# Optimization experiments

Measured on AMD Instinct MI355X. Metric: run time of the kernel, lower is better.

Reference implementation:

```python
import jax, jax.numpy as jnp
import numpy as np

D_MODEL = 1024
N_HEADS = 16
HEAD_DIM = D_MODEL // N_HEADS
NUM_SINK = 4
WINDOW = 512
B, S = 1, 4096


def _sink_visible(S):
    # visible[i, j] = (j <= i) & ((j < NUM_SINK) | (j >= i - WINDOW + 1))
    i = jnp.arange(S)[:, None]
    j = jnp.arange(S)[None, :]
    return (j <= i) & ((j < NUM_SINK) | (j >= i - WINDOW + 1))


def setup_inputs() -> dict:
    key = jax.random.key(0)
    kx, kq, kk, kv, ko = jax.random.split(key, 5)
    sc = 1.0 / np.sqrt(D_MODEL)
    return {
        "x": jax.random.normal(kx, (B, S, D_MODEL), dtype=jnp.float32),
        "Wq": jax.random.normal(kq, (D_MODEL, D_MODEL), dtype=jnp.float32) * sc,
        "Wk": jax.random.normal(kk, (D_MODEL, D_MODEL), dtype=jnp.float32) * sc,
        "Wv": jax.random.normal(kv, (D_MODEL, D_MODEL), dtype=jnp.float32) * sc,
        "Wo": jax.random.normal(ko, (D_MODEL, D_MODEL), dtype=jnp.float32) * sc,
    }


def reference(x, Wq, Wk, Wv, Wo):
    Bx, Sx, D = x.shape
    H, hd = N_HEADS, HEAD_DIM
    # nn.Linear (no bias): y = x @ W^T
    q = (x @ Wq.T).reshape(Bx, Sx, H, hd).transpose(0, 2, 1, 3)  # (B,H,S,hd)
    k = (x @ Wk.T).reshape(Bx, Sx, H, hd).transpose(0, 2, 1, 3)
    v = (x @ Wv.T).reshape(Bx, Sx, H, hd).transpose(0, 2, 1, 3)
    scale = 1.0 / np.sqrt(hd)
    scores = jnp.einsum("bhqd,bhkd->bhqk", q, k) * scale  # (B,H,S,S)
    visible = _sink_visible(Sx)  # (S,S) bool; every row has j=i visible
    scores = jnp.where(visible[None, None], scores, -jnp.inf)
    attn = jax.nn.softmax(scores, axis=-1)
    out = jnp.einsum("bhqk,bhkd->bhqd", attn, v)
    out = out.transpose(0, 2, 1, 3).reshape(Bx, Sx, D)
    return out @ Wo.T
```

## Files before the change

### kernel.cpp

```cpp
#include <hip/hip_runtime.h>
#include <stdint.h>

#define AS1 __attribute__((address_space(1)))
#define AS3 __attribute__((address_space(3)))

typedef short short8 __attribute__((ext_vector_type(8)));
typedef unsigned short ushort8 __attribute__((ext_vector_type(8)));
typedef __bf16 bf16x8 __attribute__((ext_vector_type(8)));
typedef float floatx4 __attribute__((ext_vector_type(4)));

__device__ __forceinline__ floatx4 mfma16(short8 a, short8 b, floatx4 c) {
  return __builtin_amdgcn_mfma_f32_16x16x32_bf16(
      __builtin_bit_cast(bf16x8, a), __builtin_bit_cast(bf16x8, b), c, 0, 0, 0);
}

__device__ __forceinline__ unsigned short f2bf(float f) {
  uint32_t u = __builtin_bit_cast(uint32_t, f);
  u = (u + 0x7FFFu + ((u >> 16) & 1u)) >> 16;
  return (unsigned short)u;
}

__device__ __forceinline__ uint32_t cvt_pk_bf16(float a, float b) {
  uint32_t d;
  asm("v_cvt_pk_bf16_f32 %0, %1, %2" : "=v"(d) : "v"(a), "v"(b));
  return d;
}

__global__ __launch_bounds__(256) void convert_pack(
    const float4* __restrict__ x, const float4* __restrict__ wq,
    const float4* __restrict__ wk, const float4* __restrict__ wv,
    const float4* __restrict__ wo, ushort4* __restrict__ xb,
    ushort4* __restrict__ wqkvb, ushort4* __restrict__ wob) {
  int i = blockIdx.x * 256 + threadIdx.x;
  const float4* src;
  ushort4* dst;
  if (i < (1 << 20)) {
    src = x + i;
    dst = xb + i;
  } else {
    int t = i - (1 << 20);
    int r = t >> 18;
    int j = t & ((1 << 18) - 1);
    src = (r == 0 ? wq : r == 1 ? wk : r == 2 ? wv : wo) + j;
    dst = (r < 3) ? (wqkvb + (r << 18) + j) : (wob + j);
  }
  float4 v = *src;
  ushort4 o;
  o.x = f2bf(v.x);
  o.y = f2bf(v.y);
  o.z = f2bf(v.z);
  o.w = f2bf(v.w);
  *dst = o;
}

template <typename OutT>
__global__ __launch_bounds__(256) void gemm_bt(const unsigned short* __restrict__ A,
                                               const unsigned short* __restrict__ Bm,
                                               OutT* __restrict__ C, int N, int K) {
  __shared__ unsigned short lds[3][16 * 512];
  const int tid = threadIdx.x;
  const int lane = tid & 63;
  const int w = tid >> 6;
  const int wr = w >> 1, wc = w & 1;

  const int lid = blockIdx.y * gridDim.x + blockIdx.x;
  const int xcd = lid & 7;
  const int wgid = xcd * 96 + (lid >> 3);
  const int s = wgid >> 5, w5 = wgid & 31;
  const int mt = (s & 3) * 8 + (w5 & 7);
  const int nt = (s >> 2) * 4 + (w5 >> 3);
  const int tm = mt * 128, tn = nt * 128;
  const int lrow = lane & 15;
  const int lk = (lane >> 4) * 8;

  floatx4 acc[4][4];
#pragma unroll
  for (int i = 0; i < 4; ++i)
#pragma unroll
    for (int j = 0; j < 4; ++j) acc[i][j] = floatx4{0.f, 0.f, 0.f, 0.f};

  auto stage = [&](unsigned short* buf, int k0) {
#pragma unroll
    for (int c = w * 4; c < w * 4 + 4; ++c) {
      const unsigned short* g;
      if (c < 8) {
        g = A + (size_t)(tm + c * 16 + lrow) * K + (k0 + lk);
      } else {
        g = Bm + (size_t)(tn + (c - 8) * 16 + lrow) * K + (k0 + lk);
      }
      __builtin_amdgcn_global_load_lds((const AS1 uint32_t*)g,
                                       (AS3 uint32_t*)(buf + c * 512), 16, 0, 0);
    }
  };

  auto compute = [&](const unsigned short* L) {
    short8 af[4], bf[4];
#pragma unroll
    for (int i = 0; i < 4; ++i)
      af[i] = *(const short8*)&L[(wr * 4 + i) * 512 + lane * 8];
#pragma unroll
    for (int j = 0; j < 4; ++j)
      bf[j] = *(const short8*)&L[(8 + wc * 4 + j) * 512 + lane * 8];
#pragma unroll
    for (int i = 0; i < 4; ++i)
#pragma unroll
      for (int j = 0; j < 4; ++j) acc[i][j] = mfma16(af[i], bf[j], acc[i][j]);
  };

  stage(lds[0], 0);
  stage(lds[1], 32);

  const int T = K >> 5;
  int bt = 0;
  for (int t = 0; t < T - 1; ++t) {
    asm volatile("s_waitcnt vmcnt(4)" ::: "memory");
    __builtin_amdgcn_sched_barrier(0);
    __builtin_amdgcn_s_barrier();
    __builtin_amdgcn_sched_barrier(0);
    if (t + 2 < T) {
      int b2 = (bt + 2 >= 3) ? bt - 1 : bt + 2;
      stage(lds[b2], (t + 2) << 5);
    }
    compute(lds[bt]);
    bt = (bt + 1 == 3) ? 0 : bt + 1;
  }
  asm volatile("s_waitcnt vmcnt(0)" ::: "memory");
  __builtin_amdgcn_sched_barrier(0);
  __builtin_amdgcn_s_barrier();
  __builtin_amdgcn_sched_barrier(0);
  compute(lds[bt]);

  const int r0 = (lane >> 4) * 4;
#pragma unroll
  for (int i = 0; i < 4; ++i)
#pragma unroll
    for (int j = 0; j < 4; ++j)
#pragma unroll
      for (int r = 0; r < 4; ++r) {
        int row = tm + wr * 64 + i * 16 + r0 + r;
        int col = tn + wc * 64 + j * 16 + lrow;
        float v = acc[i][j][r];
        if constexpr (sizeof(OutT) == 2)
          C[(size_t)row * N + col] = f2bf(v);
        else
          C[(size_t)row * N + col] = v;
      }
}

__global__ __launch_bounds__(256) void gemm64(const unsigned short* __restrict__ A,
                                              const unsigned short* __restrict__ Bm,
                                              float* __restrict__ C, int N, int K) {
  __shared__ unsigned short lds[3][12 * 512];
  const int tid = threadIdx.x;
  const int lane = tid & 63;
  const int w = tid >> 6;
  const int wr = w >> 1, wc = w & 1;

  const int lid = blockIdx.y * gridDim.x + blockIdx.x;
  const int xcd = lid & 7;
  const int wgid = xcd * 64 + (lid >> 3);
  const int s = wgid >> 5, w5 = wgid & 31;
  const int mt = (s & 3) * 16 + (w5 & 15);
  const int nt = (s >> 2) * 2 + (w5 >> 4);
  const int tm = mt * 64, tn = nt * 128;
  const int lrow = lane & 15;
  const int lk = (lane >> 4) * 8;

  floatx4 acc[2][4];
#pragma unroll
  for (int i = 0; i < 2; ++i)
#pragma unroll
    for (int j = 0; j < 4; ++j) acc[i][j] = floatx4{0.f, 0.f, 0.f, 0.f};

  auto stage = [&](unsigned short* buf, int k0) {
#pragma unroll
    for (int c = w * 3; c < w * 3 + 3; ++c) {
      const unsigned short* g;
      if (c < 4) {
        g = A + (size_t)(tm + c * 16 + lrow) * K + (k0 + lk);
      } else {
        g = Bm + (size_t)(tn + (c - 4) * 16 + lrow) * K + (k0 + lk);
      }
      __builtin_amdgcn_global_load_lds((const AS1 uint32_t*)g,
                                       (AS3 uint32_t*)(buf + c * 512), 16, 0, 0);
    }
  };

  auto compute = [&](const unsigned short* L) {
    short8 af[2], bf[4];
#pragma unroll
    for (int i = 0; i < 2; ++i)
      af[i] = *(const short8*)&L[(wr * 2 + i) * 512 + lane * 8];
#pragma unroll
    for (int j = 0; j < 4; ++j)
      bf[j] = *(const short8*)&L[(4 + wc * 4 + j) * 512 + lane * 8];
#pragma unroll
    for (int i = 0; i < 2; ++i)
#pragma unroll
      for (int j = 0; j < 4; ++j) acc[i][j] = mfma16(af[i], bf[j], acc[i][j]);
  };

  stage(lds[0], 0);
  stage(lds[1], 32);

  const int T = K >> 5;
  int bt = 0;
  for (int t = 0; t < T - 1; ++t) {
    asm volatile("s_waitcnt vmcnt(3)" ::: "memory");
    __builtin_amdgcn_sched_barrier(0);
    __builtin_amdgcn_s_barrier();
    __builtin_amdgcn_sched_barrier(0);
    if (t + 2 < T) {
      int b2 = (bt + 2 >= 3) ? bt - 1 : bt + 2;
      stage(lds[b2], (t + 2) << 5);
    }
    compute(lds[bt]);
    bt = (bt + 1 == 3) ? 0 : bt + 1;
  }
  asm volatile("s_waitcnt vmcnt(0)" ::: "memory");
  __builtin_amdgcn_sched_barrier(0);
  __builtin_amdgcn_s_barrier();
  __builtin_amdgcn_sched_barrier(0);
  compute(lds[bt]);

  const int r0 = (lane >> 4) * 4;
#pragma unroll
  for (int i = 0; i < 2; ++i)
#pragma unroll
    for (int j = 0; j < 4; ++j)
#pragma unroll
      for (int r = 0; r < 4; ++r) {
        int row = tm + (wr * 2 + i) * 16 + r0 + r;
        int col = tn + (wc * 4 + j) * 16 + lrow;
        C[(size_t)row * N + col] = acc[i][j][r];
      }
}

__global__ __launch_bounds__(256) void attn_kernel(const unsigned short* __restrict__ qkv,
                                                   unsigned short* __restrict__ aout) {
  __shared__ unsigned short Klds[2][16 * 512];
  __shared__ unsigned short VT[64 * 136];
  __shared__ unsigned short PT[4][16 * 136];

  const int tid = threadIdx.x;
  const int lane = tid & 63;
  const int w = tid >> 6;
  const int lrow = lane & 15;
  const int lkg = lane >> 4;

  const int i = blockIdx.x;
  const int half = i >> 8;
  const int j = (i >> 3) & 31;
  const int h = 2 * (i & 7) + half;
  const int qb = half ? (31 - j) : j;
  const int q0 = qb * 128;

  short8 qf[2][2];
#pragma unroll
  for (int qt = 0; qt < 2; ++qt)
#pragma unroll
    for (int ks = 0; ks < 2; ++ks)
      qf[qt][ks] = *(const short8*)&qkv[(size_t)(q0 + qt * 64 + w * 16 + lrow) * 3072 +
                                        h * 64 + ks * 32 + lkg * 8];

  float m_i[2], l_i[2];
  floatx4 o[4][2];
#pragma unroll
  for (int qt = 0; qt < 2; ++qt) {
    m_i[qt] = -1e30f;
    l_i[qt] = 0.f;
#pragma unroll
    for (int nt = 0; nt < 4; ++nt) o[nt][qt] = floatx4{0.f, 0.f, 0.f, 0.f};
  }

  const float scale2 = 0.125f * 1.44269504088896f;

  if (w < 2) {
    const unsigned short* g = &qkv[(size_t)lrow * 3072 + 1024 + h * 64 + w * 32 + lkg * 8];
    __builtin_amdgcn_global_load_lds((const AS1 uint32_t*)g,
                                     (AS3 uint32_t*)(&Klds[0][w * 512]), 16, 0, 0);
  }
  {
    if (lane < 16) {
      const unsigned short* g0 = &qkv[(size_t)(2 * lane) * 3072 + 2048 + h * 64 + w * 16];
      ushort8 a0 = *(const ushort8*)g0;
      ushort8 a1 = *(const ushort8*)(g0 + 8);
      ushort8 b0 = *(const ushort8*)(g0 + 3072);
      ushort8 b1 = *(const ushort8*)(g0 + 3080);
      uint32_t* vt = (uint32_t*)VT;
#pragma unroll
      for (int dd = 0; dd < 8; ++dd) {
        vt[(w * 16 + dd) * 68 + lane] = (uint32_t)a0[dd] | ((uint32_t)b0[dd] << 16);
        vt[(w * 16 + 8 + dd) * 68 + lane] = (uint32_t)a1[dd] | ((uint32_t)b1[dd] << 16);
      }
    }
  }
  const int kb0 = (q0 - 511 < 16) ? 16 : (q0 - 511);
#pragma unroll
  for (int c = 0; c < 4; ++c) {
    int ch = w * 4 + c;
    int kt = ch >> 1, ks = ch & 1;
    const unsigned short* g =
        &qkv[(size_t)(kb0 + kt * 16 + lrow) * 3072 + 1024 + h * 64 + ks * 32 + lkg * 8];
    __builtin_amdgcn_global_load_lds((const AS1 uint32_t*)g,
                                     (AS3 uint32_t*)(&Klds[1][ch * 512]), 16, 0, 0);
  }
  ushort8 va0, va1, vb0, vb1;
  {
    const unsigned short* g0 = &qkv[(size_t)(kb0 + 2 * lane) * 3072 + 2048 + h * 64 + w * 16];
    va0 = *(const ushort8*)g0;
    va1 = *(const ushort8*)(g0 + 8);
    vb0 = *(const ushort8*)(g0 + 3072);
    vb1 = *(const ushort8*)(g0 + 3080);
  }
  __syncthreads();

#pragma unroll
  for (int qt = 0; qt < 2; ++qt) {
    const int qq = q0 + qt * 64 + w * 16 + lrow;
    floatx4 s0 = floatx4{0.f, 0.f, 0.f, 0.f};
#pragma unroll
    for (int ks = 0; ks < 2; ++ks) {
      short8 kf = *(const short8*)&Klds[0][ks * 512 + lane * 8];
      s0 = mfma16(kf, qf[qt][ks], s0);
    }
    float mx = -1e30f;
    float sv[4];
#pragma unroll
    for (int r = 0; r < 4; ++r) {
      int key = lkg * 4 + r;
      bool vis = (key <= qq) && ((key < 4) || (key >= qq - 511));
      sv[r] = vis ? s0[r] * scale2 : -1e30f;
      mx = fmaxf(mx, sv[r]);
    }
    mx = fmaxf(mx, __shfl_xor(mx, 16));
    mx = fmaxf(mx, __shfl_xor(mx, 32));
    m_i[qt] = mx;
    float p0 = exp2f(sv[0] - mx), p1 = exp2f(sv[1] - mx);
    float p2 = exp2f(sv[2] - mx), p3 = exp2f(sv[3] - mx);
    float ps = (p0 + p1) + (p2 + p3);
    *(uint2*)&PT[w][lrow * 136 + lkg * 4] = uint2{cvt_pk_bf16(p0, p1), cvt_pk_bf16(p2, p3)};
    *(uint2*)&PT[w][lrow * 136 + 16 + lkg * 4] = uint2{0u, 0u};
    ps += __shfl_xor(ps, 16);
    ps += __shfl_xor(ps, 32);
    l_i[qt] = ps;
    short8 pf = *(const short8*)&PT[w][lrow * 136 + lkg * 8];
#pragma unroll
    for (int nt = 0; nt < 4; ++nt) {
      short8 vf = *(const short8*)&VT[(nt * 16 + lrow) * 136 + lkg * 8];
      o[nt][qt] = mfma16(vf, pf, o[nt][qt]);
    }
  }

  int nbuf = 1;
  for (int kb = kb0; kb < q0 + 128; kb += 128) {
    const bool hasnext = (kb + 128 < q0 + 128);
    __syncthreads();
    {
      uint32_t* vt = (uint32_t*)VT;
#pragma unroll
      for (int dd = 0; dd < 8; ++dd) {
        vt[(w * 16 + dd) * 68 + lane] = (uint32_t)va0[dd] | ((uint32_t)vb0[dd] << 16);
        vt[(w * 16 + 8 + dd) * 68 + lane] = (uint32_t)va1[dd] | ((uint32_t)vb1[dd] << 16);
      }
    }
    __syncthreads();

    if (hasnext) {
      const int kn = kb + 128;
#pragma unroll
      for (int c = 0; c < 4; ++c) {
        int ch = w * 4 + c;
        int kt = ch >> 1, ks = ch & 1;
        const unsigned short* g =
            &qkv[(size_t)(kn + kt * 16 + lrow) * 3072 + 1024 + h * 64 + ks * 32 + lkg * 8];
        __builtin_amdgcn_global_load_lds((const AS1 uint32_t*)g,
                                         (AS3 uint32_t*)(&Klds[1 - nbuf][ch * 512]), 16, 0, 0);
      }
      const unsigned short* g0 = &qkv[(size_t)(kn + 2 * lane) * 3072 + 2048 + h * 64 + w * 16];
      va0 = *(const ushort8*)g0;
      va1 = *(const ushort8*)(g0 + 8);
      vb0 = *(const ushort8*)(g0 + 3072);
      vb1 = *(const ushort8*)(g0 + 3080);
    }

#pragma unroll
    for (int qt = 0; qt < 2; ++qt) {
      const int qaT = q0 + qt * 64 + w * 16;
      const int qq = qaT + lrow;
      floatx4 s[8];
#pragma unroll
      for (int ct = 0; ct < 8; ++ct) {
        s[ct] = floatx4{0.f, 0.f, 0.f, 0.f};
#pragma unroll
        for (int ks = 0; ks < 2; ++ks) {
          short8 kf = *(const short8*)&Klds[nbuf][(ct * 2 + ks) * 512 + lane * 8];
          s[ct] = mfma16(kf, qf[qt][ks], s[ct]);
        }
      }
      const bool full = (kb + 127 <= qaT) && (kb >= qaT + 15 - 511);
      float mx = -1e30f;
#pragma unroll
      for (int ct = 0; ct < 8; ++ct)
#pragma unroll
        for (int r = 0; r < 4; ++r) {
          float val = s[ct][r] * scale2;
          if (!full) {
            int key = kb + ct * 16 + lkg * 4 + r;
            bool vis = (key <= qq) && (key >= qq - 511);
            val = vis ? val : -1e30f;
          }
          s[ct][r] = val;
          mx = fmaxf(mx, val);
        }
      mx = fmaxf(mx, __shfl_xor(mx, 16));
      mx = fmaxf(mx, __shfl_xor(mx, 32));
      float nm = fmaxf(m_i[qt], mx);
      float alpha = exp2f(m_i[qt] - nm);
      m_i[qt] = nm;

      float ps = 0.f;
#pragma unroll
      for (int ct = 0; ct < 8; ++ct) {
        float p0 = exp2f(s[ct][0] - nm), p1 = exp2f(s[ct][1] - nm);
        float p2 = exp2f(s[ct][2] - nm), p3 = exp2f(s[ct][3] - nm);
        ps += (p0 + p1) + (p2 + p3);
        *(uint2*)&PT[w][lrow * 136 + ct * 16 + lkg * 4] =
            uint2{cvt_pk_bf16(p0, p1), cvt_pk_bf16(p2, p3)};
      }
      ps += __shfl_xor(ps, 16);
      ps += __shfl_xor(ps, 32);
      l_i[qt] = l_i[qt] * alpha + ps;

#pragma unroll
      for (int nt = 0; nt < 4; ++nt)
#pragma unroll
        for (int r = 0; r < 4; ++r) o[nt][qt][r] *= alpha;

#pragma unroll
      for (int kk = 0; kk < 4; ++kk) {
        short8 pf = *(const short8*)&PT[w][lrow * 136 + kk * 32 + lkg * 8];
#pragma unroll
        for (int nt = 0; nt < 4; ++nt) {
          short8 vf = *(const short8*)&VT[(nt * 16 + lrow) * 136 + kk * 32 + lkg * 8];
          o[nt][qt] = mfma16(vf, pf, o[nt][qt]);
        }
      }
    }
    nbuf ^= 1;
  }

#pragma unroll
  for (int qt = 0; qt < 2; ++qt) {
    const int qq = q0 + qt * 64 + w * 16 + lrow;
    const float inv = 1.0f / l_i[qt];
#pragma unroll
    for (int nt = 0; nt < 4; ++nt) {
      floatx4 ov = o[nt][qt];
      uint32_t lo = cvt_pk_bf16(ov[0] * inv, ov[1] * inv);
      uint32_t hi = cvt_pk_bf16(ov[2] * inv, ov[3] * inv);
      *(uint2*)&aout[(size_t)qq * 1024 + h * 64 + nt * 16 + lkg * 4] = uint2{lo, hi};
    }
  }
}

extern "C" void kernel_launch(void* const* d_in, const int* in_sizes, int n_in,
                              void* d_out, int out_size, void* d_ws, size_t ws_size,
                              hipStream_t stream) {
  const float* x = (const float*)d_in[0];
  const float* wq = (const float*)d_in[1];
  const float* wk = (const float*)d_in[2];
  const float* wv = (const float*)d_in[3];
  const float* wo = (const float*)d_in[4];

  char* ws = (char*)d_ws;
  unsigned short* Xb = (unsigned short*)(ws);
  unsigned short* Wqkv = (unsigned short*)(ws + (8u << 20));
  unsigned short* Wob = (unsigned short*)(ws + (14u << 20));
  unsigned short* QKV = (unsigned short*)(ws + (16u << 20));
  unsigned short* AO = (unsigned short*)(ws + (40u << 20));

  convert_pack<<<8192, 256, 0, stream>>>((const float4*)x, (const float4*)wq,
                                         (const float4*)wk, (const float4*)wv,
                                         (const float4*)wo, (ushort4*)Xb,
                                         (ushort4*)Wqkv, (ushort4*)Wob);
  gemm_bt<unsigned short><<<dim3(32, 24), 256, 0, stream>>>(Xb, Wqkv, QKV, 3072, 1024);
  attn_kernel<<<512, 256, 0, stream>>>(QKV, AO);
  gemm64<<<dim3(64, 8), 256, 0, stream>>>(AO, Wob, (float*)d_out, 1024, 1024);
}
```

Measured before the change: 193.4 us.

## Pre-tile bf16 operands so GEMM stages load contiguous 1KB chunks

The conversion kernel now writes X, Wqkv and Wo in bf16 into a tiled layout that matches the LDS staging order (128-row tile, 32-wide k-step, 16-row chunk), eight elements per thread. The GEMM staging then reads one contiguous 1KB block per chunk instead of 16 strided row segments, which should improve global load coalescing. The output GEMM keeps row-major AO but reads the tiled Wo. This adds index math to the conversion kernel, and its scattered 16-byte stores may cost more there.

```diff
diff --git a/kernel.cpp b/kernel.cpp
--- a/kernel.cpp
+++ b/kernel.cpp
@@ -26,31 +26,47 @@
   return d;
 }
 
+__device__ __forceinline__ size_t tiled_off(int row, int col) {
+  int rt = row >> 7, c8 = (row >> 4) & 7, rr = row & 15;
+  int t = col >> 5, lh = (col >> 3) & 3, e = col & 7;
+  return ((size_t)((rt * 32 + t) * 8 + c8) << 9) + (lh * 16 + rr) * 8 + e;
+}
+
 __global__ __launch_bounds__(256) void convert_pack(
     const float4* __restrict__ x, const float4* __restrict__ wq,
     const float4* __restrict__ wk, const float4* __restrict__ wv,
-    const float4* __restrict__ wo, ushort4* __restrict__ xb,
-    ushort4* __restrict__ wqkvb, ushort4* __restrict__ wob) {
+    const float4* __restrict__ wo, unsigned short* __restrict__ xb,
+    unsigned short* __restrict__ wqkvb, unsigned short* __restrict__ wob) {
   int i = blockIdx.x * 256 + threadIdx.x;
   const float4* src;
-  ushort4* dst;
-  if (i < (1 << 20)) {
-    src = x + i;
-    dst = xb + i;
+  unsigned short* dstbase;
+  int row, cb;
+  if (i < (1 << 19)) {
+    row = i >> 7;
+    cb = i & 127;
+    src = x + row * 256 + cb * 2;
+    dstbase = xb + tiled_off(row, cb * 8);
+  } else if (i < 917504) {
+    int j = i - (1 << 19);
+    int r = j >> 17;
+    int jj = j & 131071;
+    int rw = jj >> 7;
+    cb = jj & 127;
+    src = (r == 0 ? wq : r == 1 ? wk : wv) + rw * 256 + cb * 2;
+    row = r * 1024 + rw;
+    dstbase = wqkvb + tiled_off(row, cb * 8);
   } else {
-    int t = i - (1 << 20);
-    int r = t >> 18;
-    int j = t & ((1 << 18) - 1);
-    src = (r == 0 ? wq : r == 1 ? wk : r == 2 ? wv : wo) + j;
-    dst = (r < 3) ? (wqkvb + (r << 18) + j) : (wob + j);
-  }
-  float4 v = *src;
-  ushort4 o;
-  o.x = f2bf(v.x);
-  o.y = f2bf(v.y);
-  o.z = f2bf(v.z);
-  o.w = f2bf(v.w);
-  *dst = o;
+    int j = i - 917504;
+    row = j >> 7;
+    cb = j & 127;
+    src = wo + row * 256 + cb * 2;
+    dstbase = wob + tiled_off(row, cb * 8);
+  }
+  float4 a = src[0], b = src[1];
+  ushort8 o;
+  o[0] = f2bf(a.x); o[1] = f2bf(a.y); o[2] = f2bf(a.z); o[3] = f2bf(a.w);
+  o[4] = f2bf(b.x); o[5] = f2bf(b.y); o[6] = f2bf(b.z); o[7] = f2bf(b.w);
+  *(ushort8*)dstbase = o;
 }
 
 template <typename OutT>
@@ -71,7 +87,6 @@
   const int nt = (s >> 2) * 4 + (w5 >> 3);
   const int tm = mt * 128, tn = nt * 128;
   const int lrow = lane & 15;
-  const int lk = (lane >> 4) * 8;
 
   floatx4 acc[4][4];
 #pragma unroll
@@ -79,15 +94,14 @@
 #pragma unroll
     for (int j = 0; j < 4; ++j) acc[i][j] = floatx4{0.f, 0.f, 0.f, 0.f};
 
-  auto stage = [&](unsigned short* buf, int k0) {
+  auto stage = [&](unsigned short* buf, int t) {
 #pragma unroll
     for (int c = w * 4; c < w * 4 + 4; ++c) {
       const unsigned short* g;
-      if (c < 8) {
-        g = A + (size_t)(tm + c * 16 + lrow) * K + (k0 + lk);
-      } else {
-        g = Bm + (size_t)(tn + (c - 8) * 16 + lrow) * K + (k0 + lk);
-      }
+      if (c < 8)
+        g = A + ((size_t)((mt * 32 + t) * 8 + c) << 9) + lane * 8;
+      else
+        g = Bm + ((size_t)((nt * 32 + t) * 8 + (c - 8)) << 9) + lane * 8;
       __builtin_amdgcn_global_load_lds((const AS1 uint32_t*)g,
                                        (AS3 uint32_t*)(buf + c * 512), 16, 0, 0);
     }
@@ -108,7 +122,7 @@
   };
 
   stage(lds[0], 0);
-  stage(lds[1], 32);
+  stage(lds[1], 1);
 
   const int T = K >> 5;
   int bt = 0;
@@ -119,7 +133,7 @@
     __builtin_amdgcn_sched_barrier(0);
     if (t + 2 < T) {
       int b2 = (bt + 2 >= 3) ? bt - 1 : bt + 2;
-      stage(lds[b2], (t + 2) << 5);
+      stage(lds[b2], t + 2);
     }
     compute(lds[bt]);
     bt = (bt + 1 == 3) ? 0 : bt + 1;
@@ -172,14 +186,14 @@
 #pragma unroll
     for (int j = 0; j < 4; ++j) acc[i][j] = floatx4{0.f, 0.f, 0.f, 0.f};
 
-  auto stage = [&](unsigned short* buf, int k0) {
+  auto stage = [&](unsigned short* buf, int t) {
 #pragma unroll
     for (int c = w * 3; c < w * 3 + 3; ++c) {
       const unsigned short* g;
       if (c < 4) {
-        g = A + (size_t)(tm + c * 16 + lrow) * K + (k0 + lk);
+        g = A + (size_t)(tm + c * 16 + lrow) * K + (t * 32 + lk);
       } else {
-        g = Bm + (size_t)(tn + (c - 4) * 16 + lrow) * K + (k0 + lk);
+        g = Bm + ((size_t)((nt * 32 + t) * 8 + (c - 4)) << 9) + lane * 8;
       }
       __builtin_amdgcn_global_load_lds((const AS1 uint32_t*)g,
                                        (AS3 uint32_t*)(buf + c * 512), 16, 0, 0);
@@ -201,7 +215,7 @@
   };
 
   stage(lds[0], 0);
-  stage(lds[1], 32);
+  stage(lds[1], 1);
 
   const int T = K >> 5;
   int bt = 0;
@@ -212,7 +226,7 @@
     __builtin_amdgcn_sched_barrier(0);
     if (t + 2 < T) {
       int b2 = (bt + 2 >= 3) ? bt - 1 : bt + 2;
-      stage(lds[b2], (t + 2) << 5);
+      stage(lds[b2], t + 2);
     }
     compute(lds[bt]);
     bt = (bt + 1 == 3) ? 0 : bt + 1;
@@ -480,10 +494,9 @@
   unsigned short* QKV = (unsigned short*)(ws + (16u << 20));
   unsigned short* AO = (unsigned short*)(ws + (40u << 20));
 
-  convert_pack<<<8192, 256, 0, stream>>>((const float4*)x, (const float4*)wq,
+  convert_pack<<<4096, 256, 0, stream>>>((const float4*)x, (const float4*)wq,
                                          (const float4*)wk, (const float4*)wv,
-                                         (const float4*)wo, (ushort4*)Xb,
-                                         (ushort4*)Wqkv, (ushort4*)Wob);
+                                         (const float4*)wo, Xb, Wqkv, Wob);
   gemm_bt<unsigned short><<<dim3(32, 24), 256, 0, stream>>>(Xb, Wqkv, QKV, 3072, 1024);
   attn_kernel<<<512, 256, 0, stream>>>(QKV, AO);
   gemm64<<<dim3(64, 8), 256, 0, stream>>>(AO, Wob, (float*)d_out, 1024, 1024);
```

Result: faster. 171.8 us (-11.1%).
